# Kernel optimization log

Measured on AMD Instinct MI355X. Metric: run time of the kernel, lower is better.

Reference implementation:

```python
import jax, jax.numpy as jnp
import numpy as np

TEMPERATURE = 1.0
STRIDE = 1
PADDING = 2
RF = 5  # receptive_field_size
TREE_DEPTH = 3

# Each of the 16 binary difflogic ops op_g(a,b) is multilinear:
# op_g = c0 + c1*a + c2*b + c3*a*b. Rows ordered per the standard difflogic table:
# 0:0, 1:a&b, 2:a&~b, 3:a, 4:~a&b, 5:b, 6:xor, 7:or, 8:nor, 9:xnor,
# 10:~b, 11:a|~b, 12:~a, 13:~a|b, 14:nand, 15:1
_C = jnp.asarray(np.array([
    [0, 0, 0, 0],
    [0, 0, 0, 1],
    [0, 1, 0, -1],
    [0, 1, 0, 0],
    [0, 0, 1, -1],
    [0, 0, 1, 0],
    [0, 1, 1, -2],
    [0, 1, 1, -1],
    [1, -1, -1, 1],
    [1, -1, -1, 2],
    [1, 0, -1, 0],
    [1, 0, -1, 1],
    [1, -1, 0, 0],
    [1, -1, 0, 1],
    [1, 0, 0, -1],
    [1, 0, 0, 0]], dtype=np.float32))


def _gate(a, b, logits):
    """Soft LUT gate. a,b: (B,K,N,P); logits: (N,K,16) -> (B,K,N,P)."""
    w = jax.nn.softmax(logits / TEMPERATURE, axis=-1)          # (N,K,16)
    coef = jnp.einsum('nkg,gc->knc', w, _C)                    # (K,N,4)
    c = coef[None, :, :, None, :]                              # (1,K,N,1,4)
    return c[..., 0] + c[..., 1] * a + c[..., 2] * b + c[..., 3] * (a * b)


def setup_inputs() -> dict:
    key = jax.random.key(0)
    ks = jax.random.split(key, 8)
    B, Cin, H, W = 16, 32, 64, 64
    K, N = 64, 2 ** TREE_DEPTH  # num_kernels, leaf gates per tree
    x = jax.random.uniform(ks[0], (B, Cin, H, W), dtype=jnp.float32)
    idx_h = jax.random.randint(ks[1], (2, K, N), 0, RF, dtype=jnp.int32)
    idx_w = jax.random.randint(ks[2], (2, K, N), 0, RF, dtype=jnp.int32)
    idx_c = jax.random.randint(ks[3], (2, K, N), 0, Cin, dtype=jnp.int32)
    w0 = jax.random.normal(ks[4], (8, K, 16), dtype=jnp.float32)
    w1 = jax.random.normal(ks[5], (4, K, 16), dtype=jnp.float32)
    w2 = jax.random.normal(ks[6], (2, K, 16), dtype=jnp.float32)
    w3 = jax.random.normal(ks[7], (1, K, 16), dtype=jnp.float32)
    return {"x": x, "idx_h": idx_h, "idx_w": idx_w, "idx_c": idx_c,
            "w0": w0, "w1": w1, "w2": w2, "w3": w3}


def reference(x, idx_h, idx_w, idx_c, w0, w1, w2, w3):
    B, Cin, H, W = x.shape
    xp = jnp.pad(x, ((0, 0), (0, 0), (PADDING, PADDING), (PADDING, PADDING)))
    out_h = (H + 2 * PADDING - RF) // STRIDE + 1
    out_w = (W + 2 * PADDING - RF) // STRIDE + 1
    # Absolute gather coords per (rank-slot, kernel, leaf-gate, out_y, out_x)
    abs_h = idx_h[..., None, None] + (jnp.arange(out_h) * STRIDE)[:, None]   # (2,K,N,oh,1)
    abs_w = idx_w[..., None, None] + (jnp.arange(out_w) * STRIDE)[None, :]   # (2,K,N,1,ow)
    cc = idx_c[..., None, None]                                              # (2,K,N,1,1)
    g = xp[:, cc, abs_h, abs_w]                                # (B,2,K,N,oh,ow)
    K, N = g.shape[2], g.shape[3]
    g = g.reshape(B, 2, K, N, out_h * out_w)                   # (B,2,K,N,P)
    cur = _gate(g[:, 0], g[:, 1], w0)                          # (B,K,8,P) leaf level
    for wl in (w1, w2, w3):                                    # reduce tree: 8->4->2->1
        cur = _gate(cur[:, :, 0::2, :], cur[:, :, 1::2, :], wl)
    return cur.reshape(B, K, out_h, out_w)
```

## Files before the change

### kernel.cpp

```cpp
#include <hip/hip_runtime.h>
#include <hip/hip_bf16.h>

#define CIN 32
#define HW 64
#define KK 64
#define NLEAF 8
#define PADDING 2
#define TH 4
#define TCW 16
#define WR 8
#define WC 20
#define WPOS (CIN * WR * WC)

typedef float f32x2 __attribute__((ext_vector_type(2)));
typedef float f32x4 __attribute__((ext_vector_type(4)));

__device__ __constant__ float d_C[16][4] = {
    {0, 0, 0, 0},  {0, 0, 0, 1},  {0, 1, 0, -1}, {0, 1, 0, 0},
    {0, 0, 1, -1}, {0, 0, 1, 0},  {0, 1, 1, -2}, {0, 1, 1, -1},
    {1, -1, -1, 1},{1, -1, -1, 2},{1, 0, -1, 0}, {1, 0, -1, 1},
    {1, -1, 0, 0}, {1, -1, 0, 1}, {1, 0, 0, -1}, {1, 0, 0, 0}
};

__global__ __launch_bounds__(256) void prep_kernel(
    const int* __restrict__ idx_h, const int* __restrict__ idx_w, const int* __restrict__ idx_c,
    const float* __restrict__ w0, const float* __restrict__ w1,
    const float* __restrict__ w2, const float* __restrict__ w3,
    float* __restrict__ coefA, int* __restrict__ loffA)
{
    int tid = blockIdx.x * 256 + threadIdx.x;

    {
        int k = tid >> 4, n = tid & 15;
        int s = n >> 3, leaf = n & 7;
        int o = s * (KK * NLEAF) + k * NLEAF + leaf;
        loffA[tid] = idx_c[o] * (WR * WC) + idx_h[o] * WC + idx_w[o];
        (void)k;
    }

    if (tid < KK * 15) {
        int k = tid / 15, node = tid % 15;
        const float* wp; int n;
        if (node < 8)       { wp = w0; n = node; }
        else if (node < 12) { wp = w1; n = node - 8; }
        else if (node < 14) { wp = w2; n = node - 12; }
        else                { wp = w3; n = 0; }
        const float4* lp = (const float4*)(wp + (size_t)(n * KK + k) * 16);
        float4 L0 = lp[0], L1 = lp[1], L2 = lp[2], L3 = lp[3];
        float l[16] = {L0.x, L0.y, L0.z, L0.w, L1.x, L1.y, L1.z, L1.w,
                       L2.x, L2.y, L2.z, L2.w, L3.x, L3.y, L3.z, L3.w};
        float m = l[0];
        #pragma unroll
        for (int g = 1; g < 16; ++g) m = fmaxf(m, l[g]);
        float p[16], s = 0.f;
        #pragma unroll
        for (int g = 0; g < 16; ++g) { p[g] = __expf(l[g] - m); s += p[g]; }
        float inv = 1.f / s;
        float c0 = 0, c1 = 0, c2 = 0, c3 = 0;
        #pragma unroll
        for (int g = 0; g < 16; ++g) {
            float w = p[g] * inv;
            c0 = fmaf(w, d_C[g][0], c0);
            c1 = fmaf(w, d_C[g][1], c1);
            c2 = fmaf(w, d_C[g][2], c2);
            c3 = fmaf(w, d_C[g][3], c3);
        }
        float* o = coefA + (k * 60 + node * 4);
        o[0] = c0; o[1] = c1; o[2] = c2; o[3] = c3;
    }
}

__device__ __forceinline__ f32x2 bc(float s) { return (f32x2){s, s}; }
__device__ __forceinline__ f32x2 gate2(const float* c, f32x2 a, f32x2 b) {
    return __builtin_elementwise_fma(b,
               __builtin_elementwise_fma(a, bc(c[3]), bc(c[2])),
               __builtin_elementwise_fma(a, bc(c[1]), bc(c[0])));
}

__global__ __launch_bounds__(512, 4) void logic_conv_kernel(
    const float* __restrict__ x, const int* __restrict__ loffA,
    const float* __restrict__ coefA, float* __restrict__ out)
{
    extern __shared__ f32x4 xt[];

    int tid  = threadIdx.x;
    int grp  = blockIdx.x & 7;
    int quad = grp & 3;
    int kh   = grp >> 2;
    int t    = blockIdx.x >> 3;
    int r0   = (t >> 2) * TH;
    int c0   = (t & 3) * TCW;

    const float* xb0 = x + (size_t)(4 * quad) * (CIN * HW * HW);
    const float* xb1 = xb0 + (CIN * HW * HW);
    const float* xb2 = xb1 + (CIN * HW * HW);
    const float* xb3 = xb2 + (CIN * HW * HW);

    #pragma unroll
    for (int i = 0; i < 10; ++i) {
        int e  = tid + i * 512;
        int c  = e / (WR * WC);
        int r  = e - c * (WR * WC);
        int rr = r / WC;
        int cc = r - rr * WC;
        int ih = r0 + rr - PADDING, iw = c0 + cc - PADDING;
        f32x4 v = {0.f, 0.f, 0.f, 0.f};
        if ((unsigned)ih < HW && (unsigned)iw < HW) {
            int go = (c * HW + ih) * HW + iw;
            v.x = xb0[go];
            v.y = xb1[go];
            v.z = xb2[go];
            v.w = xb3[go];
        }
        xt[e] = v;
    }
    __syncthreads();

    int lane = tid & 63, wave = tid >> 6;
    int tr = lane >> 4, tc = lane & 15;
    int pxe   = tr * WC + tc;
    int pxout = (r0 + tr) * HW + (c0 + tc);
    float* outB0 = out + ((size_t)(4 * quad) << 18);
    float* outB1 = outB0 + (1 << 18);
    float* outB2 = outB1 + (1 << 18);
    float* outB3 = outB2 + (1 << 18);

    int kbase = __builtin_amdgcn_readfirstlane(kh * 32 + wave * 4);

    #pragma unroll 2
    for (int i = 0; i < 4; ++i) {
        int k = kbase + i;
        const int*   L = loffA + (k << 4);
        const float* C = coefA + k * 60;

        f32x2 gA[16], gB[16];
        #pragma unroll
        for (int n = 0; n < 16; ++n) {
            f32x4 gv = xt[L[n] + pxe];
            gA[n] = (f32x2){gv.x, gv.y};
            gB[n] = (f32x2){gv.z, gv.w};
        }

        f32x2 vA[8], vB[8];
        #pragma unroll
        for (int n = 0; n < 8; ++n) {
            vA[n] = gate2(C + 4 * n, gA[n], gA[8 + n]);
            vB[n] = gate2(C + 4 * n, gB[n], gB[8 + n]);
        }
        f32x2 uA[4], uB[4];
        #pragma unroll
        for (int n = 0; n < 4; ++n) {
            uA[n] = gate2(C + 32 + 4 * n, vA[2 * n], vA[2 * n + 1]);
            uB[n] = gate2(C + 32 + 4 * n, vB[2 * n], vB[2 * n + 1]);
        }
        f32x2 sA0 = gate2(C + 48, uA[0], uA[1]);
        f32x2 sA1 = gate2(C + 52, uA[2], uA[3]);
        f32x2 sB0 = gate2(C + 48, uB[0], uB[1]);
        f32x2 sB1 = gate2(C + 52, uB[2], uB[3]);
        f32x2 qA  = gate2(C + 56, sA0, sA1);
        f32x2 qB  = gate2(C + 56, sB0, sB1);

        int ko = (k << 12) + pxout;
        __builtin_nontemporal_store(qA.x, &outB0[ko]);
        __builtin_nontemporal_store(qA.y, &outB1[ko]);
        __builtin_nontemporal_store(qB.x, &outB2[ko]);
        __builtin_nontemporal_store(qB.y, &outB3[ko]);
    }
}

extern "C" void kernel_launch(void* const* d_in, const int* in_sizes, int n_in,
                              void* d_out, int out_size, void* d_ws, size_t ws_size,
                              hipStream_t stream) {
    const float* x     = (const float*)d_in[0];
    const int*   idx_h = (const int*)d_in[1];
    const int*   idx_w = (const int*)d_in[2];
    const int*   idx_c = (const int*)d_in[3];
    const float* w0    = (const float*)d_in[4];
    const float* w1    = (const float*)d_in[5];
    const float* w2    = (const float*)d_in[6];
    const float* w3    = (const float*)d_in[7];
    float* out   = (float*)d_out;

    float* coefA = (float*)d_ws;
    int*   loffA = (int*)((char*)d_ws + 16384);

    hipLaunchKernelGGL(prep_kernel, dim3(4), dim3(256), 0, stream,
                       idx_h, idx_w, idx_c, w0, w1, w2, w3, coefA, loffA);
    hipLaunchKernelGGL(logic_conv_kernel, dim3(512), dim3(512),
                       WPOS * sizeof(f32x4), stream,
                       x, loffA, coefA, out);
}
```

Measured before the change: 21.26 us.

## Pack per-kernel offsets and coefficients into one blob and broadcast via readlane

```diff
diff --git a/kernel.cpp b/kernel.cpp
--- a/kernel.cpp
+++ b/kernel.cpp
@@ -26,7 +26,7 @@
     const int* __restrict__ idx_h, const int* __restrict__ idx_w, const int* __restrict__ idx_c,
     const float* __restrict__ w0, const float* __restrict__ w1,
     const float* __restrict__ w2, const float* __restrict__ w3,
-    float* __restrict__ coefA, int* __restrict__ loffA)
+    float* __restrict__ blob)
 {
     int tid = blockIdx.x * 256 + threadIdx.x;
 
@@ -34,8 +34,8 @@
         int k = tid >> 4, n = tid & 15;
         int s = n >> 3, leaf = n & 7;
         int o = s * (KK * NLEAF) + k * NLEAF + leaf;
-        loffA[tid] = idx_c[o] * (WR * WC) + idx_h[o] * WC + idx_w[o];
-        (void)k;
+        ((int*)blob)[k * 80 + n] =
+            (idx_c[o] * (WR * WC) + idx_h[o] * WC + idx_w[o]) * 16;
     }
 
     if (tid < KK * 15) {
@@ -65,21 +65,22 @@
             c2 = fmaf(w, d_C[g][2], c2);
             c3 = fmaf(w, d_C[g][3], c3);
         }
-        float* o = coefA + (k * 60 + node * 4);
+        float* o = blob + (k * 80 + 16 + node * 4);
         o[0] = c0; o[1] = c1; o[2] = c2; o[3] = c3;
     }
 }
 
 __device__ __forceinline__ f32x2 bc(float s) { return (f32x2){s, s}; }
-__device__ __forceinline__ f32x2 gate2(const float* c, f32x2 a, f32x2 b) {
+__device__ __forceinline__ f32x2 gate2s(float c0, float c1, float c2, float c3,
+                                        f32x2 a, f32x2 b) {
     return __builtin_elementwise_fma(b,
-               __builtin_elementwise_fma(a, bc(c[3]), bc(c[2])),
-               __builtin_elementwise_fma(a, bc(c[1]), bc(c[0])));
+               __builtin_elementwise_fma(a, bc(c3), bc(c2)),
+               __builtin_elementwise_fma(a, bc(c1), bc(c0)));
 }
 
 __global__ __launch_bounds__(512, 4) void logic_conv_kernel(
-    const float* __restrict__ x, const int* __restrict__ loffA,
-    const float* __restrict__ coefA, float* __restrict__ out)
+    const float* __restrict__ x, const float* __restrict__ blob,
+    float* __restrict__ out)
 {
     extern __shared__ f32x4 xt[];
 
@@ -91,6 +92,16 @@
     int r0   = (t >> 2) * TH;
     int c0   = (t & 3) * TCW;
 
+    int lane = tid & 63, wave = tid >> 6;
+    int kbase = __builtin_amdgcn_readfirstlane(kh * 32 + wave * 4);
+
+    unsigned cc[5];
+    {
+        const unsigned* bu = (const unsigned*)blob + kbase * 80 + lane;
+        #pragma unroll
+        for (int i = 0; i < 5; ++i) cc[i] = bu[i * 64];
+    }
+
     const float* xb0 = x + (size_t)(4 * quad) * (CIN * HW * HW);
     const float* xb1 = xb0 + (CIN * HW * HW);
     const float* xb2 = xb1 + (CIN * HW * HW);
@@ -102,8 +113,8 @@
         int c  = e / (WR * WC);
         int r  = e - c * (WR * WC);
         int rr = r / WC;
-        int cc = r - rr * WC;
-        int ih = r0 + rr - PADDING, iw = c0 + cc - PADDING;
+        int cc2 = r - rr * WC;
+        int ih = r0 + rr - PADDING, iw = c0 + cc2 - PADDING;
         f32x4 v = {0.f, 0.f, 0.f, 0.f};
         if ((unsigned)ih < HW && (unsigned)iw < HW) {
             int go = (c * HW + ih) * HW + iw;
@@ -116,27 +127,27 @@
     }
     __syncthreads();
 
-    int lane = tid & 63, wave = tid >> 6;
     int tr = lane >> 4, tc = lane & 15;
-    int pxe   = tr * WC + tc;
+    int pxb   = (tr * WC + tc) * 16;
     int pxout = (r0 + tr) * HW + (c0 + tc);
     float* outB0 = out + ((size_t)(4 * quad) << 18);
     float* outB1 = outB0 + (1 << 18);
     float* outB2 = outB1 + (1 << 18);
     float* outB3 = outB2 + (1 << 18);
-
-    int kbase = __builtin_amdgcn_readfirstlane(kh * 32 + wave * 4);
+    const char* xtb = (const char*)xt;
+
+#define RL(i)  __builtin_amdgcn_readlane(cc[(D + (i)) >> 6], (D + (i)) & 63)
+#define RLF(i) __uint_as_float(RL(i))
 
     #pragma unroll 2
-    for (int i = 0; i < 4; ++i) {
-        int k = kbase + i;
-        const int*   L = loffA + (k << 4);
-        const float* C = coefA + k * 60;
+    for (int j = 0; j < 4; ++j) {
+        const int D = j * 80;
 
         f32x2 gA[16], gB[16];
         #pragma unroll
         for (int n = 0; n < 16; ++n) {
-            f32x4 gv = xt[L[n] + pxe];
+            int off = (int)RL(n);
+            f32x4 gv = *(const f32x4*)(xtb + (off + pxb));
             gA[n] = (f32x2){gv.x, gv.y};
             gB[n] = (f32x2){gv.z, gv.w};
         }
@@ -144,28 +155,37 @@
         f32x2 vA[8], vB[8];
         #pragma unroll
         for (int n = 0; n < 8; ++n) {
-            vA[n] = gate2(C + 4 * n, gA[n], gA[8 + n]);
-            vB[n] = gate2(C + 4 * n, gB[n], gB[8 + n]);
+            float c0v = RLF(16 + 4 * n), c1v = RLF(17 + 4 * n);
+            float c2v = RLF(18 + 4 * n), c3v = RLF(19 + 4 * n);
+            vA[n] = gate2s(c0v, c1v, c2v, c3v, gA[n], gA[8 + n]);
+            vB[n] = gate2s(c0v, c1v, c2v, c3v, gB[n], gB[8 + n]);
         }
         f32x2 uA[4], uB[4];
         #pragma unroll
         for (int n = 0; n < 4; ++n) {
-            uA[n] = gate2(C + 32 + 4 * n, vA[2 * n], vA[2 * n + 1]);
-            uB[n] = gate2(C + 32 + 4 * n, vB[2 * n], vB[2 * n + 1]);
-        }
-        f32x2 sA0 = gate2(C + 48, uA[0], uA[1]);
-        f32x2 sA1 = gate2(C + 52, uA[2], uA[3]);
-        f32x2 sB0 = gate2(C + 48, uB[0], uB[1]);
-        f32x2 sB1 = gate2(C + 52, uB[2], uB[3]);
-        f32x2 qA  = gate2(C + 56, sA0, sA1);
-        f32x2 qB  = gate2(C + 56, sB0, sB1);
-
-        int ko = (k << 12) + pxout;
+            float c0v = RLF(48 + 4 * n), c1v = RLF(49 + 4 * n);
+            float c2v = RLF(50 + 4 * n), c3v = RLF(51 + 4 * n);
+            uA[n] = gate2s(c0v, c1v, c2v, c3v, vA[2 * n], vA[2 * n + 1]);
+            uB[n] = gate2s(c0v, c1v, c2v, c3v, vB[2 * n], vB[2 * n + 1]);
+        }
+        float e0 = RLF(64), e1 = RLF(65), e2 = RLF(66), e3 = RLF(67);
+        f32x2 sA0 = gate2s(e0, e1, e2, e3, uA[0], uA[1]);
+        f32x2 sB0 = gate2s(e0, e1, e2, e3, uB[0], uB[1]);
+        float f0 = RLF(68), f1 = RLF(69), f2 = RLF(70), f3 = RLF(71);
+        f32x2 sA1 = gate2s(f0, f1, f2, f3, uA[2], uA[3]);
+        f32x2 sB1 = gate2s(f0, f1, f2, f3, uB[2], uB[3]);
+        float h0 = RLF(72), h1 = RLF(73), h2 = RLF(74), h3 = RLF(75);
+        f32x2 qA = gate2s(h0, h1, h2, h3, sA0, sA1);
+        f32x2 qB = gate2s(h0, h1, h2, h3, sB0, sB1);
+
+        int ko = ((kbase + j) << 12) + pxout;
         __builtin_nontemporal_store(qA.x, &outB0[ko]);
         __builtin_nontemporal_store(qA.y, &outB1[ko]);
         __builtin_nontemporal_store(qB.x, &outB2[ko]);
         __builtin_nontemporal_store(qB.y, &outB3[ko]);
     }
+#undef RL
+#undef RLF
 }
 
 extern "C" void kernel_launch(void* const* d_in, const int* in_sizes, int n_in,
@@ -179,14 +199,12 @@
     const float* w1    = (const float*)d_in[5];
     const float* w2    = (const float*)d_in[6];
     const float* w3    = (const float*)d_in[7];
-    float* out   = (float*)d_out;
-
-    float* coefA = (float*)d_ws;
-    int*   loffA = (int*)((char*)d_ws + 16384);
+    float* out  = (float*)d_out;
+    float* blob = (float*)d_ws;
 
     hipLaunchKernelGGL(prep_kernel, dim3(4), dim3(256), 0, stream,
-                       idx_h, idx_w, idx_c, w0, w1, w2, w3, coefA, loffA);
+                       idx_h, idx_w, idx_c, w0, w1, w2, w3, blob);
     hipLaunchKernelGGL(logic_conv_kernel, dim3(512), dim3(512),
                        WPOS * sizeof(f32x4), stream,
-                       x, loffA, coefA, out);
-}
+                       x, blob, out);
+}
```

Measured after the change: 41.10 us. +93.3%, slower.
